# Performance work log

Measured on AMD Instinct MI355X. Metric: run time of the kernel, lower is better.

The kernel has to match this reference:

```python
import jax, jax.numpy as jnp
import numpy as np

# Model constants (match init_kwargs)
L = 32              # one_side_length (effective_L)
ED = 32             # embed_dim = n_ssm (repeat = 1)
ND = 2              # ndim
DIR = 4             # directions_amount
KD = DIR * ED       # kernel_dim = 128
R = 2 * L ** 3      # coeff_matrix_row_amount = 65536
V = 2 * L           # power_dim = 64
SCALE = (1.0 / ND) ** 0.5
B_IMG, H_IMG = 8, 64


def setup_inputs() -> dict:
    key = jax.random.key(0)
    ks = jax.random.split(key, 24)
    inp = {}
    inp['x'] = jax.random.normal(ks[0], (B_IMG, H_IMG, H_IMG, ED), jnp.float32)
    i = 1
    for d in ('h', 'v'):
        for s in ('A1', 'A2', 'A3', 'A4'):
            inp[f'M{d}_{s}'] = jax.random.uniform(ks[i], (R, V), jnp.float32); i += 1
        inp[f'M{d}_B'] = jax.random.uniform(ks[i], (R, 2), jnp.float32); i += 1
    for p in ('A_1', 'A_2', 'A_3', 'A_4', 'B_1', 'B_2', 'C_1', 'C_2'):
        inp[p] = jax.random.normal(ks[i], (KD, ND), jnp.float32); i += 1
    inp['W'] = jax.random.normal(ks[i], (ED, ED), jnp.float32); i += 1
    inp['b'] = jnp.zeros((ED,), jnp.float32)
    return inp


def _compute_kernel(Ms_h, Ms_v, A_list, B_1, B_2, C_1, C_2):
    # A powers via exp/log trick: [V, KD, ND]
    ell = jnp.arange(V, dtype=jnp.float32)
    Apow = [jnp.exp(ell[:, None, None] * jnp.log(jax.nn.sigmoid(a))[None]) for a in A_list]
    Bstk = jnp.stack([jax.nn.sigmoid(B_1), jax.nn.sigmoid(B_2)], 0)  # [2, KD, ND]
    vecs = Apow + [Bstk]
    outs = []
    for Ms in (Ms_h, Ms_v):
        prod = None
        for M, vec in zip(Ms, vecs):
            cur = jnp.einsum('rv,vhn->rhn', M, vec)  # [R, KD, ND]
            prod = cur if prod is None else prod * cur
        # [L^2, R/L^2, KD, ND] -> sum over r2 -> [L^2, KD, ND]
        outs.append(prod.reshape(L * L, R // (L * L), KD, ND).sum(axis=1))
    out = (jnp.einsum('lhn,hn->lh', outs[0], C_1 * SCALE)
           + jnp.einsum('lhn,hn->lh', outs[1], C_2 * SCALE))
    out = out.reshape(L, L, KD)
    # boundary corrections (first row/col doubled, corner net-unchanged)
    out = out.at[0, :, :].multiply(2.0)
    out = out.at[:, 0, :].multiply(2.0)
    out = out.at[0, 0].divide(4.0)
    return out  # [L, L, KD]


def _forward(x, Ms_h, Ms_v, A_list, B_1, B_2, C_1, C_2, W, b):
    xc = jnp.transpose(x, (0, 3, 1, 2))  # b c h w  (transpose=True path)
    H = xc.shape[-1]
    k = jnp.transpose(_compute_kernel(Ms_h, Ms_v, A_list, B_1, B_2, C_1, C_2), (2, 0, 1))  # [KD, L, L]
    pad = H - L
    k = jnp.pad(k, ((0, 0), (0, pad), (0, pad)))  # [KD, H, H]
    s2 = (2 * H, 2 * H)
    flips = [(), (2,), (3,), (2, 3)]
    y = None
    for i, fl in enumerate(flips):
        ki = k[i * ED:(i + 1) * ED]  # [ED, H, H] (repeat == 1)
        xi = jnp.flip(xc, fl) if fl else xc
        xf = jnp.fft.rfft2(xi, s=s2)
        kf = jnp.fft.rfft2(ki, s=s2)
        cur = jnp.fft.irfft2(xf * kf, s=s2)[..., :H, :H]
        cur = jnp.flip(cur, fl) if fl else cur
        y = cur if y is None else y + cur
    y = jnp.transpose(y, (0, 2, 3, 1))  # b h w c
    return y @ W.T + b  # mixing linear layer on channels


def reference(x, Mh_A1, Mh_A2, Mh_A3, Mh_A4, Mh_B,
              Mv_A1, Mv_A2, Mv_A3, Mv_A4, Mv_B,
              A_1, A_2, A_3, A_4, B_1, B_2, C_1, C_2, W, b):
    Ms_h = (Mh_A1, Mh_A2, Mh_A3, Mh_A4, Mh_B)
    Ms_v = (Mv_A1, Mv_A2, Mv_A3, Mv_A4, Mv_B)
    return _forward(x, Ms_h, Ms_v, [A_1, A_2, A_3, A_4], B_1, B_2, C_1, C_2, W, b)
```

## Files before the change

### kernel.cpp

```cpp
#include <hip/hip_runtime.h>
#include <hip/hip_fp16.h>

typedef _Float16 f16x8 __attribute__((ext_vector_type(8)));
typedef _Float16 half4v __attribute__((ext_vector_type(4)));
typedef float float4v __attribute__((ext_vector_type(4)));
typedef __attribute__((ext_vector_type(8))) short short8;
typedef __attribute__((ext_vector_type(16))) float f32x16;

#define WS_BFH   0
#define WS_BSG   65536
#define WS_OUTS  66048
#define WS_KC    590336
#define WS_XPAD  719360
#define WS_YC    1767936
#define WS_TF    2816512

__device__ inline unsigned short f2bf(float f) {
  unsigned int u = __float_as_uint(f);
  u += 0x7fffu + ((u >> 16) & 1u);
  return (unsigned short)(u >> 16);
}

__global__ void k0_prep(const float* __restrict__ A1, const float* __restrict__ A2,
                        const float* __restrict__ A3, const float* __restrict__ A4,
                        const float* __restrict__ B1, const float* __restrict__ B2,
                        _Float16* __restrict__ Bfh, float* __restrict__ bsg) {
  const int blk = blockIdx.x;
  const int i = blk >> 1, kb = blk & 1;
  const int hn = threadIdx.x;
  const float* As[4] = {A1, A2, A3, A4};
  const float a = As[i][hn];
  const float s = 1.0f / (1.0f + expf(-a));
  float p = 1.0f;
  for (int v = 0; v < kb * 32; ++v) p *= s;
  const int ntile = hn >> 4;
  #pragma unroll
  for (int g = 0; g < 4; ++g) {
    _Float16 h[8];
    #pragma unroll
    for (int j = 0; j < 8; ++j) { h[j] = (_Float16)p; p *= s; }
    const int lane = (hn & 15) | (g << 4);
    _Float16* dst = Bfh + ((((i * 2 + kb) * 16 + ntile) * 64 + lane) << 3);
    *(f16x8*)dst = *(f16x8*)h;
  }
  if (blk == 0) {
    bsg[hn]       = 1.0f / (1.0f + expf(-B1[hn]));
    bsg[256 + hn] = 1.0f / (1.0f + expf(-B2[hn]));
  }
}

__global__ __launch_bounds__(256, 4) void k1_mfma(
    const float* __restrict__ Mh0, const float* __restrict__ Mh1,
    const float* __restrict__ Mh2, const float* __restrict__ Mh3,
    const float* __restrict__ MhB,
    const float* __restrict__ Mv0, const float* __restrict__ Mv1,
    const float* __restrict__ Mv2, const float* __restrict__ Mv3,
    const float* __restrict__ MvB,
    const _Float16* __restrict__ Bfh, const float* __restrict__ bsg,
    float* __restrict__ outs) {
  __shared__ _Float16 Alds[4 * 4 * 2 * 64 * 8];
  __shared__ float MBs[128];
  __shared__ float bsgs[512];

  const int bd = blockIdx.x >> 10;
  const int l  = blockIdx.x & 1023;
  const float* Ms[4] = {bd ? Mv0 : Mh0, bd ? Mv1 : Mh1, bd ? Mv2 : Mh2, bd ? Mv3 : Mh3};
  const float* MB    = bd ? MvB : MhB;
  const int t = threadIdx.x;

  if (t < 128) MBs[t] = MB[l * 128 + t];
  bsgs[t]       = bsg[t];
  bsgs[256 + t] = bsg[256 + t];

  float4 st[16];
  #pragma unroll
  for (int i = 0; i < 4; ++i) {
    const float* M = Ms[i] + l * 4096;
    #pragma unroll
    for (int c0 = 0; c0 < 4; ++c0) {
      const int c = t + c0 * 256;
      st[i * 4 + c0] = *(const float4*)(M + ((c >> 4) * 64) + ((c & 15) << 2));
    }
  }
  #pragma unroll
  for (int i = 0; i < 4; ++i)
    #pragma unroll
    for (int c0 = 0; c0 < 4; ++c0) {
      const int c = t + c0 * 256;
      const int row = c >> 4;
      const int v4  = (c & 15) << 2;
      const int m     = row >> 4;
      const int lane2 = (row & 15) | (((v4 >> 3) & 3) << 4);
      const int kb    = v4 >> 5;
      const int jj    = v4 & 7;
      const float4 f = st[i * 4 + c0];
      half4v* dst = (half4v*)&Alds[((((i * 4 + m) * 2 + kb) * 64 + lane2) << 3) + jj];
      *dst = (half4v){(_Float16)f.x, (_Float16)f.y, (_Float16)f.z, (_Float16)f.w};
    }
  __syncthreads();

  const int w    = t >> 6;
  const int lane = t & 63;
  const int q = lane >> 4, col = lane & 15;

  #pragma unroll
  for (int half = 0; half < 2; ++half) {
    float4v E[4][2];
    #pragma unroll
    for (int i = 0; i < 4; ++i) {
      float4v acc[4][2];
      #pragma unroll
      for (int m = 0; m < 4; ++m)
        #pragma unroll
        for (int n = 0; n < 2; ++n) acc[m][n] = (float4v){0.f, 0.f, 0.f, 0.f};
      f16x8 Bf[2][2];
      #pragma unroll
      for (int kb = 0; kb < 2; ++kb)
        #pragma unroll
        for (int n = 0; n < 2; ++n)
          Bf[kb][n] = *(const f16x8*)(Bfh +
              ((((i * 2 + kb) * 16 + (w * 4 + half * 2 + n)) * 64 + lane) << 3));
      #pragma unroll
      for (int kb = 0; kb < 2; ++kb)
        #pragma unroll
        for (int m = 0; m < 4; ++m) {
          const f16x8 Af = *(const f16x8*)&Alds[((((i * 4 + m) * 2 + kb) * 64 + lane) << 3)];
          #pragma unroll
          for (int n = 0; n < 2; ++n)
            acc[m][n] = __builtin_amdgcn_mfma_f32_16x16x32_f16(Af, Bf[kb][n], acc[m][n], 0, 0, 0);
        }
      if (i == 0) {
        #pragma unroll
        for (int m = 0; m < 4; ++m)
          #pragma unroll
          for (int n = 0; n < 2; ++n) E[m][n] = acc[m][n];
      } else {
        #pragma unroll
        for (int m = 0; m < 4; ++m)
          #pragma unroll
          for (int n = 0; n < 2; ++n) E[m][n] *= acc[m][n];
      }
    }

    #pragma unroll
    for (int n = 0; n < 2; ++n) {
      const int hn = w * 64 + (half * 2 + n) * 16 + col;
      const float b0 = bsgs[hn], b1 = bsgs[256 + hn];
      float ssum = 0.f;
      #pragma unroll
      for (int m = 0; m < 4; ++m)
        #pragma unroll
        for (int r = 0; r < 4; ++r) {
          const int row = m * 16 + q * 4 + r;
          const float bdot = MBs[row * 2] * b0 + MBs[row * 2 + 1] * b1;
          ssum = fmaf(E[m][n][r], bdot, ssum);
        }
      ssum += __shfl_xor(ssum, 16);
      ssum += __shfl_xor(ssum, 32);
      if (lane < 16) outs[(bd * 1024 + l) * 256 + hn] = ssum;
    }
  }
}

__global__ void k2_kc(const float* __restrict__ outs, const float* __restrict__ C1,
                      const float* __restrict__ C2, float* __restrict__ kc) {
  const int c = blockIdx.x >> 3;
  const int base = (blockIdx.x & 7) * 504;
  const float SC = 0.70710678118654752f;
  for (int idx = base + threadIdx.x; idx < base + 504 && idx < 63 * 64; idx += 256) {
    const int U = idx >> 6, V = idx & 63;
    float acc = 0.f;
    if (V < 63) {
      const int u = U - 31, v = V - 31;
      #pragma unroll
      for (int d = 0; d < 4; ++d) {
        const int dy = (d == 1 || d == 3) ? u : -u;
        const int dx = (d == 2 || d == 3) ? v : -v;
        if (dy >= 0 && dy < 32 && dx >= 0 && dx < 32) {
          const int l = dy * 32 + dx;
          const int h = d * 32 + c;
          const float e = (dy == 0 && dx == 0) ? 1.f : ((dy == 0 || dx == 0) ? 2.f : 1.f);
          const float s0 = outs[l * 256 + h * 2 + 0] * C1[h * 2 + 0]
                         + outs[l * 256 + h * 2 + 1] * C1[h * 2 + 1];
          const float s1 = outs[262144 + l * 256 + h * 2 + 0] * C2[h * 2 + 0]
                         + outs[262144 + l * 256 + h * 2 + 1] * C2[h * 2 + 1];
          acc += e * SC * (s0 + s1);
        }
      }
    }
    kc[(c * 63 + U) * 64 + V] = acc;
  }
}

__global__ void k2b_tfrag(const float* __restrict__ kc, unsigned short* __restrict__ Tf) {
  const int cu = blockIdx.x;
  const float* kcr = kc + cu * 64;
  const int t = threadIdx.x;
  #pragma unroll
  for (int s = 0; s < 2; ++s) {
    const int slot = t + s * 256;
    const int f = slot >> 6, lane = slot & 63;
    const int kt = f >> 1, nt = f & 1;
    const int kbase = kt * 16 + (lane >> 5) * 8;
    const int n = nt * 32 + (lane & 31);
    unsigned int o[4];
    #pragma unroll
    for (int jp = 0; jp < 4; ++jp) {
      unsigned short h0, h1;
      {
        const int v = (kbase + 2 * jp) - n + 31;
        h0 = (v >= 0 && v < 63) ? f2bf(kcr[v]) : 0;
      }
      {
        const int v = (kbase + 2 * jp + 1) - n + 31;
        h1 = (v >= 0 && v < 63) ? f2bf(kcr[v]) : 0;
      }
      o[jp] = (unsigned int)h0 | ((unsigned int)h1 << 16);
    }
    unsigned int* dst = (unsigned int*)(Tf + (cu * 8 + f) * 512 + lane * 8);
    dst[0] = o[0]; dst[1] = o[1]; dst[2] = o[2]; dst[3] = o[3];
  }
}

__global__ void k3_xt(const float* __restrict__ x, unsigned short* __restrict__ Xpad) {
  __shared__ float ls[4 * 64 * 33];
  const int b = blockIdx.x >> 4, pt = blockIdx.x & 15;
  const int t = threadIdx.x;
  const float* src = x + (b * 64 + pt * 4) * 2048;
  #pragma unroll 8
  for (int k = 0; k < 32; ++k) {
    const int e = t + k * 256;
    const int p = e >> 11, q = (e >> 5) & 63, cl = e & 31;
    ls[(p * 64 + q) * 33 + cl] = src[e];
  }
  unsigned int* Xp32 = (unsigned int*)Xpad;
  for (int idx = blockIdx.x * 3968 + t; idx < (blockIdx.x + 1) * 3968; idx += 256) {
    const int seg = idx / 992, off = idx - seg * 992;
    const int bb = seg >> 6, cc = (seg >> 1) & 31, hf = seg & 1;
    Xp32[(bb * 32 + cc) * 4032 + (hf ? 3040 : 0) + off] = 0u;
  }
  __syncthreads();
  #pragma unroll 8
  for (int k = 0; k < 16; ++k) {
    const int o = t + k * 256;
    const int cl = o >> 7, p = (o >> 5) & 3, q2 = o & 31;
    const float f0 = ls[(p * 64 + 2 * q2 + 0) * 33 + cl];
    const float f1 = ls[(p * 64 + 2 * q2 + 1) * 33 + cl];
    const unsigned int pk = (unsigned int)f2bf(f0) | ((unsigned int)f2bf(f1) << 16);
    Xp32[(b * 32 + cl) * 4032 + (pt * 4 + p + 31) * 32 + q2] = pk;
  }
}

__global__ __launch_bounds__(256, 2) void k4b_conv(const unsigned short* __restrict__ Xpad,
                                                   const unsigned short* __restrict__ Tf,
                                                   float* __restrict__ yc) {
  __shared__ float red[4 * 4096];
  const int bc = blockIdx.x;
  const int c  = bc & 31;
  const int t = threadIdx.x, w = t >> 6, lane = t & 63;
  const unsigned short* Xp = Xpad + bc * 8064;
  const unsigned short* Tc = Tf + c * 63 * 4096;
  const int r = lane & 31, kh = lane >> 5;

  f32x16 acc[2][2];
  #pragma unroll
  for (int m = 0; m < 2; ++m)
    #pragma unroll
    for (int n = 0; n < 2; ++n)
      #pragma unroll
      for (int e = 0; e < 16; ++e) acc[m][n][e] = 0.f;

  short8 Ac[2][4], Bc[4][2];
  int u = w;
  #pragma unroll
  for (int m = 0; m < 2; ++m)
    #pragma unroll
    for (int kt = 0; kt < 4; ++kt)
      Ac[m][kt] = *(const short8*)(Xp + (m * 32 + r + u) * 64 + kt * 16 + kh * 8);
  #pragma unroll
  for (int kt = 0; kt < 4; ++kt)
    #pragma unroll
    for (int nt = 0; nt < 2; ++nt)
      Bc[kt][nt] = *(const short8*)(Tc + (u * 8 + kt * 2 + nt) * 512 + lane * 8);

  for (int i = 0; i < 16; ++i) {
    const int un = u + 4;
    const bool has_next = (un < 63);
    short8 An[2][4], Bn[4][2];
    if (has_next) {
      #pragma unroll
      for (int m = 0; m < 2; ++m)
        #pragma unroll
        for (int kt = 0; kt < 4; ++kt)
          An[m][kt] = *(const short8*)(Xp + (m * 32 + r + un) * 64 + kt * 16 + kh * 8);
      #pragma unroll
      for (int kt = 0; kt < 4; ++kt)
        #pragma unroll
        for (int nt = 0; nt < 2; ++nt)
          Bn[kt][nt] = *(const short8*)(Tc + (un * 8 + kt * 2 + nt) * 512 + lane * 8);
    }
    #pragma unroll
    for (int kt = 0; kt < 4; ++kt)
      #pragma unroll
      for (int m = 0; m < 2; ++m)
        #pragma unroll
        for (int nt = 0; nt < 2; ++nt)
          acc[m][nt] = __builtin_amdgcn_mfma_f32_32x32x16_bf16(Ac[m][kt], Bc[kt][nt],
                                                               acc[m][nt], 0, 0, 0);
    if (!has_next) break;
    #pragma unroll
    for (int m = 0; m < 2; ++m)
      #pragma unroll
      for (int kt = 0; kt < 4; ++kt) Ac[m][kt] = An[m][kt];
    #pragma unroll
    for (int kt = 0; kt < 4; ++kt)
      #pragma unroll
      for (int nt = 0; nt < 2; ++nt) Bc[kt][nt] = Bn[kt][nt];
    u = un;
  }

  float* my = red + w * 4096;
  #pragma unroll
  for (int m = 0; m < 2; ++m)
    #pragma unroll
    for (int nt = 0; nt < 2; ++nt)
      #pragma unroll
      for (int e = 0; e < 16; ++e) {
        const int row = (e & 3) + 8 * (e >> 2) + 4 * kh;
        my[(m * 32 + row) * 64 + nt * 32 + r] = acc[m][nt][e];
      }
  __syncthreads();
  float* out = yc + bc * 4096;
  #pragma unroll
  for (int k = 0; k < 16; ++k) {
    const int idx = t + k * 256;
    out[idx] = red[idx] + red[4096 + idx] + red[8192 + idx] + red[12288 + idx];
  }
}

__global__ void k5_out(const float* __restrict__ yc, const float* __restrict__ W,
                       const float* __restrict__ bias, float* __restrict__ out) {
  __shared__ float ysh[64 * 33];
  const int b = blockIdx.x >> 6, p = blockIdx.x & 63;
  const int t = threadIdx.x;
  const float* ybp = yc + b * 131072 + p * 64;
  #pragma unroll
  for (int k = 0; k < 8; ++k) {
    const int f = t + k * 256;
    const int cch = f >> 6, q = f & 63;
    ysh[q * 33 + cch] = ybp[cch * 4096 + q];
  }
  const int e = t & 31;
  float wr[32];
  #pragma unroll
  for (int c4 = 0; c4 < 8; ++c4) {
    const float4 f4 = *(const float4*)(W + e * 32 + c4 * 4);
    wr[c4 * 4 + 0] = f4.x; wr[c4 * 4 + 1] = f4.y;
    wr[c4 * 4 + 2] = f4.z; wr[c4 * 4 + 3] = f4.w;
  }
  const float bb = bias[e];
  __syncthreads();
  const int q0 = t >> 5;
  #pragma unroll
  for (int k = 0; k < 8; ++k) {
    const int q = q0 + k * 8;
    float a = bb;
    #pragma unroll
    for (int cc = 0; cc < 32; ++cc) a = fmaf(ysh[q * 33 + cc], wr[cc], a);
    out[((b * 64 + p) * 64 + q) * 32 + e] = a;
  }
}

extern "C" void kernel_launch(void* const* d_in, const int* in_sizes, int n_in,
                              void* d_out, int out_size, void* d_ws, size_t ws_size,
                              hipStream_t stream) {
  const float* x   = (const float*)d_in[0];
  const float* Mh[5] = {(const float*)d_in[1], (const float*)d_in[2], (const float*)d_in[3],
                        (const float*)d_in[4], (const float*)d_in[5]};
  const float* Mv[5] = {(const float*)d_in[6], (const float*)d_in[7], (const float*)d_in[8],
                        (const float*)d_in[9], (const float*)d_in[10]};
  const float* A1 = (const float*)d_in[11];
  const float* A2 = (const float*)d_in[12];
  const float* A3 = (const float*)d_in[13];
  const float* A4 = (const float*)d_in[14];
  const float* B1 = (const float*)d_in[15];
  const float* B2 = (const float*)d_in[16];
  const float* C1 = (const float*)d_in[17];
  const float* C2 = (const float*)d_in[18];
  const float* W  = (const float*)d_in[19];
  const float* bb = (const float*)d_in[20];
  float* ws  = (float*)d_ws;
  _Float16* Bfh = (_Float16*)(ws + WS_BFH);
  float* bsg  = ws + WS_BSG;
  float* outs = ws + WS_OUTS;
  float* kc   = ws + WS_KC;
  unsigned short* Xpad = (unsigned short*)(ws + WS_XPAD);
  float* yc   = ws + WS_YC;
  unsigned short* Tf = (unsigned short*)(ws + WS_TF);

  k0_prep<<<8, 256, 0, stream>>>(A1, A2, A3, A4, B1, B2, Bfh, bsg);
  k3_xt<<<128, 256, 0, stream>>>(x, Xpad);
  k1_mfma<<<2048, 256, 0, stream>>>(Mh[0], Mh[1], Mh[2], Mh[3], Mh[4],
                                    Mv[0], Mv[1], Mv[2], Mv[3], Mv[4],
                                    Bfh, bsg, outs);
  k2_kc<<<256, 256, 0, stream>>>(outs, C1, C2, kc);
  k2b_tfrag<<<2016, 256, 0, stream>>>(kc, Tf);
  k4b_conv<<<256, 256, 0, stream>>>(Xpad, Tf, yc);
  k5_out<<<512, 256, 0, stream>>>(yc, W, bb, (float*)d_out);
}
```

Before: 253.7 us.

## Double-buffer M tiles in LDS and overlap global loads with MFMA

Replaces the up-front load of all four M matrices into a 32KB LDS tile with a two-slot 16KB ping-pong buffer. Each of the eight (half, i) steps prefetches the next M slice from global memory into registers while MFMAs run on the current slot. This cuts LDS use and register staging, which may raise occupancy and hide load latency. The cost is a barrier per step and reloading the M matrices twice, once per half.

```diff
diff --git a/kernel.cpp b/kernel.cpp
--- a/kernel.cpp
+++ b/kernel.cpp
@@ -58,7 +58,7 @@
     const float* __restrict__ MvB,
     const _Float16* __restrict__ Bfh, const float* __restrict__ bsg,
     float* __restrict__ outs) {
-  __shared__ _Float16 Alds[4 * 4 * 2 * 64 * 8];
+  __shared__ _Float16 Ai[2][4096];
   __shared__ float MBs[128];
   __shared__ float bsgs[512];
 
@@ -72,92 +72,106 @@
   bsgs[t]       = bsg[t];
   bsgs[256 + t] = bsg[256 + t];
 
-  float4 st[16];
-  #pragma unroll
-  for (int i = 0; i < 4; ++i) {
-    const float* M = Ms[i] + l * 4096;
-    #pragma unroll
-    for (int c0 = 0; c0 < 4; ++c0) {
-      const int c = t + c0 * 256;
-      st[i * 4 + c0] = *(const float4*)(M + ((c >> 4) * 64) + ((c & 15) << 2));
-    }
-  }
-  #pragma unroll
-  for (int i = 0; i < 4; ++i)
-    #pragma unroll
-    for (int c0 = 0; c0 < 4; ++c0) {
-      const int c = t + c0 * 256;
-      const int row = c >> 4;
-      const int v4  = (c & 15) << 2;
-      const int m     = row >> 4;
-      const int lane2 = (row & 15) | (((v4 >> 3) & 3) << 4);
-      const int kb    = v4 >> 5;
-      const int jj    = v4 & 7;
-      const float4 f = st[i * 4 + c0];
-      half4v* dst = (half4v*)&Alds[((((i * 4 + m) * 2 + kb) * 64 + lane2) << 3) + jj];
-      *dst = (half4v){(_Float16)f.x, (_Float16)f.y, (_Float16)f.z, (_Float16)f.w};
-    }
-  __syncthreads();
-
-  const int w    = t >> 6;
-  const int lane = t & 63;
+  const int w = t >> 6, lane = t & 63;
   const int q = lane >> 4, col = lane & 15;
 
-  #pragma unroll
-  for (int half = 0; half < 2; ++half) {
-    float4v E[4][2];
-    #pragma unroll
-    for (int i = 0; i < 4; ++i) {
-      float4v acc[4][2];
+  int loff[4];
+  #pragma unroll
+  for (int c0 = 0; c0 < 4; ++c0) {
+    const int c = t + c0 * 256;
+    const int row = c >> 4;
+    const int v4  = (c & 15) << 2;
+    loff[c0] = (((row >> 4) * 2 + (v4 >> 5)) * 64 +
+                ((row & 15) | (((v4 >> 3) & 3) << 4))) * 8 + (v4 & 7);
+  }
+  const int gbase = l * 4096 + t * 4;
+
+  {
+    float4 f[4];
+    #pragma unroll
+    for (int c0 = 0; c0 < 4; ++c0) f[c0] = *(const float4*)(Ms[0] + gbase + c0 * 1024);
+    #pragma unroll
+    for (int c0 = 0; c0 < 4; ++c0)
+      *(half4v*)&Ai[0][loff[c0]] =
+          (half4v){(_Float16)f[c0].x, (_Float16)f[c0].y, (_Float16)f[c0].z, (_Float16)f[c0].w};
+  }
+
+  float4v E[4][2];
+  #pragma unroll
+  for (int hi = 0; hi < 8; ++hi) {
+    const int half = hi >> 2, i = hi & 3;
+    __syncthreads();
+
+    float4 ldn[4];
+    if (hi < 7) {
+      const float* Mn = Ms[(hi + 1) & 3];
+      #pragma unroll
+      for (int c0 = 0; c0 < 4; ++c0) ldn[c0] = *(const float4*)(Mn + gbase + c0 * 1024);
+    }
+
+    f16x8 Bf[2][2];
+    #pragma unroll
+    for (int kb = 0; kb < 2; ++kb)
+      #pragma unroll
+      for (int n = 0; n < 2; ++n)
+        Bf[kb][n] = *(const f16x8*)(Bfh +
+            ((((i * 2 + kb) * 16 + (w * 4 + half * 2 + n)) * 64 + lane) << 3));
+
+    float4v acc[4][2];
+    #pragma unroll
+    for (int m = 0; m < 4; ++m)
+      #pragma unroll
+      for (int n = 0; n < 2; ++n) acc[m][n] = (float4v){0.f, 0.f, 0.f, 0.f};
+
+    const _Float16* Ab = &Ai[hi & 1][0];
+    #pragma unroll
+    for (int kb = 0; kb < 2; ++kb)
+      #pragma unroll
+      for (int m = 0; m < 4; ++m) {
+        const f16x8 Af = *(const f16x8*)&Ab[(((m * 2 + kb) * 64 + lane) << 3)];
+        #pragma unroll
+        for (int n = 0; n < 2; ++n)
+          acc[m][n] = __builtin_amdgcn_mfma_f32_16x16x32_f16(Af, Bf[kb][n], acc[m][n], 0, 0, 0);
+      }
+
+    if (i == 0) {
       #pragma unroll
       for (int m = 0; m < 4; ++m)
         #pragma unroll
-        for (int n = 0; n < 2; ++n) acc[m][n] = (float4v){0.f, 0.f, 0.f, 0.f};
-      f16x8 Bf[2][2];
-      #pragma unroll
-      for (int kb = 0; kb < 2; ++kb)
-        #pragma unroll
-        for (int n = 0; n < 2; ++n)
-          Bf[kb][n] = *(const f16x8*)(Bfh +
-              ((((i * 2 + kb) * 16 + (w * 4 + half * 2 + n)) * 64 + lane) << 3));
-      #pragma unroll
-      for (int kb = 0; kb < 2; ++kb)
-        #pragma unroll
-        for (int m = 0; m < 4; ++m) {
-          const f16x8 Af = *(const f16x8*)&Alds[((((i * 4 + m) * 2 + kb) * 64 + lane) << 3)];
-          #pragma unroll
-          for (int n = 0; n < 2; ++n)
-            acc[m][n] = __builtin_amdgcn_mfma_f32_16x16x32_f16(Af, Bf[kb][n], acc[m][n], 0, 0, 0);
-        }
-      if (i == 0) {
+        for (int n = 0; n < 2; ++n) E[m][n] = acc[m][n];
+    } else {
+      #pragma unroll
+      for (int m = 0; m < 4; ++m)
+        #pragma unroll
+        for (int n = 0; n < 2; ++n) E[m][n] *= acc[m][n];
+    }
+
+    if (hi < 7) {
+      #pragma unroll
+      for (int c0 = 0; c0 < 4; ++c0)
+        *(half4v*)&Ai[(hi + 1) & 1][loff[c0]] =
+            (half4v){(_Float16)ldn[c0].x, (_Float16)ldn[c0].y,
+                     (_Float16)ldn[c0].z, (_Float16)ldn[c0].w};
+    }
+
+    if (i == 3) {
+      #pragma unroll
+      for (int n = 0; n < 2; ++n) {
+        const int hn = w * 64 + (half * 2 + n) * 16 + col;
+        const float b0 = bsgs[hn], b1 = bsgs[256 + hn];
+        float ssum = 0.f;
         #pragma unroll
         for (int m = 0; m < 4; ++m)
           #pragma unroll
-          for (int n = 0; n < 2; ++n) E[m][n] = acc[m][n];
-      } else {
-        #pragma unroll
-        for (int m = 0; m < 4; ++m)
-          #pragma unroll
-          for (int n = 0; n < 2; ++n) E[m][n] *= acc[m][n];
-      }
-    }
-
-    #pragma unroll
-    for (int n = 0; n < 2; ++n) {
-      const int hn = w * 64 + (half * 2 + n) * 16 + col;
-      const float b0 = bsgs[hn], b1 = bsgs[256 + hn];
-      float ssum = 0.f;
-      #pragma unroll
-      for (int m = 0; m < 4; ++m)
-        #pragma unroll
-        for (int r = 0; r < 4; ++r) {
-          const int row = m * 16 + q * 4 + r;
-          const float bdot = MBs[row * 2] * b0 + MBs[row * 2 + 1] * b1;
-          ssum = fmaf(E[m][n][r], bdot, ssum);
-        }
-      ssum += __shfl_xor(ssum, 16);
-      ssum += __shfl_xor(ssum, 32);
-      if (lane < 16) outs[(bd * 1024 + l) * 256 + hn] = ssum;
+          for (int r = 0; r < 4; ++r) {
+            const int row = m * 16 + q * 4 + r;
+            const float bdot = MBs[row * 2] * b0 + MBs[row * 2 + 1] * b1;
+            ssum = fmaf(E[m][n][r], bdot, ssum);
+          }
+        ssum += __shfl_xor(ssum, 16);
+        ssum += __shfl_xor(ssum, 32);
+        if (lane < 16) outs[(bd * 1024 + l) * 256 + hn] = ssum;
+      }
     }
   }
 }
```

After: 262.1 us. +3.3%, slower.

## Load MFMA A-fragments directly from global memory, bypassing LDS staging

Applied to the files above, without the earlier changes.

The k1 kernel no longer stages the M coefficient matrices through shared memory. Each wave now loads its A fragments straight from global memory into registers, converts them to fp16 in registers, and computes all four N tiles in one pass instead of two halves. This removes the LDS write/read round trip and one barrier, and each wave issues the MFMAs for one i directly. In exchange every wave redundantly reads the same M rows (4x global/L2 traffic), register pressure rises, and the launch bound drops to 2 blocks per CU.

```diff
diff --git a/kernel.cpp b/kernel.cpp
--- a/kernel.cpp
+++ b/kernel.cpp
@@ -49,7 +49,7 @@
   }
 }
 
-__global__ __launch_bounds__(256, 4) void k1_mfma(
+__global__ __launch_bounds__(256, 2) void k1_mfma(
     const float* __restrict__ Mh0, const float* __restrict__ Mh1,
     const float* __restrict__ Mh2, const float* __restrict__ Mh3,
     const float* __restrict__ MhB,
@@ -58,7 +58,6 @@
     const float* __restrict__ MvB,
     const _Float16* __restrict__ Bfh, const float* __restrict__ bsg,
     float* __restrict__ outs) {
-  __shared__ _Float16 Alds[4 * 4 * 2 * 64 * 8];
   __shared__ float MBs[128];
   __shared__ float bsgs[512];
 
@@ -71,94 +70,74 @@
   if (t < 128) MBs[t] = MB[l * 128 + t];
   bsgs[t]       = bsg[t];
   bsgs[256 + t] = bsg[256 + t];
-
-  float4 st[16];
+  __syncthreads();
+
+  const int w = t >> 6, lane = t & 63;
+  const int g = lane >> 4, cc = lane & 15;
+
+  const int goff = (l * 64 + cc) * 64 + g * 8;
+
+  float4v E[4][4];
   #pragma unroll
   for (int i = 0; i < 4; ++i) {
-    const float* M = Ms[i] + l * 4096;
-    #pragma unroll
-    for (int c0 = 0; c0 < 4; ++c0) {
-      const int c = t + c0 * 256;
-      st[i * 4 + c0] = *(const float4*)(M + ((c >> 4) * 64) + ((c & 15) << 2));
+    const float* Mi = Ms[i] + goff;
+    float4 Ld[16];
+    #pragma unroll
+    for (int m = 0; m < 4; ++m)
+      #pragma unroll
+      for (int kb = 0; kb < 2; ++kb) {
+        Ld[m * 4 + kb * 2 + 0] = *(const float4*)(Mi + m * 1024 + kb * 32);
+        Ld[m * 4 + kb * 2 + 1] = *(const float4*)(Mi + m * 1024 + kb * 32 + 4);
+      }
+    f16x8 Bf[2][4];
+    #pragma unroll
+    for (int kb = 0; kb < 2; ++kb)
+      #pragma unroll
+      for (int n = 0; n < 4; ++n)
+        Bf[kb][n] = *(const f16x8*)(Bfh +
+            ((((i * 2 + kb) * 16 + (w * 4 + n)) * 64 + lane) << 3));
+
+    #pragma unroll
+    for (int m = 0; m < 4; ++m) {
+      const float4 a = Ld[m * 4 + 0], b = Ld[m * 4 + 1];
+      const float4 c = Ld[m * 4 + 2], d = Ld[m * 4 + 3];
+      const f16x8 A0 = {(_Float16)a.x, (_Float16)a.y, (_Float16)a.z, (_Float16)a.w,
+                        (_Float16)b.x, (_Float16)b.y, (_Float16)b.z, (_Float16)b.w};
+      const f16x8 A1 = {(_Float16)c.x, (_Float16)c.y, (_Float16)c.z, (_Float16)c.w,
+                        (_Float16)d.x, (_Float16)d.y, (_Float16)d.z, (_Float16)d.w};
+      float4v tn[4];
+      #pragma unroll
+      for (int n = 0; n < 4; ++n) {
+        tn[n] = __builtin_amdgcn_mfma_f32_16x16x32_f16(A0, Bf[0][n],
+                                                       (float4v){0.f, 0.f, 0.f, 0.f}, 0, 0, 0);
+        tn[n] = __builtin_amdgcn_mfma_f32_16x16x32_f16(A1, Bf[1][n], tn[n], 0, 0, 0);
+      }
+      if (i == 0) {
+        #pragma unroll
+        for (int n = 0; n < 4; ++n) E[m][n] = tn[n];
+      } else {
+        #pragma unroll
+        for (int n = 0; n < 4; ++n) E[m][n] *= tn[n];
+      }
     }
   }
-  #pragma unroll
-  for (int i = 0; i < 4; ++i)
-    #pragma unroll
-    for (int c0 = 0; c0 < 4; ++c0) {
-      const int c = t + c0 * 256;
-      const int row = c >> 4;
-      const int v4  = (c & 15) << 2;
-      const int m     = row >> 4;
-      const int lane2 = (row & 15) | (((v4 >> 3) & 3) << 4);
-      const int kb    = v4 >> 5;
-      const int jj    = v4 & 7;
-      const float4 f = st[i * 4 + c0];
-      half4v* dst = (half4v*)&Alds[((((i * 4 + m) * 2 + kb) * 64 + lane2) << 3) + jj];
-      *dst = (half4v){(_Float16)f.x, (_Float16)f.y, (_Float16)f.z, (_Float16)f.w};
-    }
-  __syncthreads();
-
-  const int w    = t >> 6;
-  const int lane = t & 63;
-  const int q = lane >> 4, col = lane & 15;
-
-  #pragma unroll
-  for (int half = 0; half < 2; ++half) {
-    float4v E[4][2];
-    #pragma unroll
-    for (int i = 0; i < 4; ++i) {
-      float4v acc[4][2];
-      #pragma unroll
-      for (int m = 0; m < 4; ++m)
-        #pragma unroll
-        for (int n = 0; n < 2; ++n) acc[m][n] = (float4v){0.f, 0.f, 0.f, 0.f};
-      f16x8 Bf[2][2];
-      #pragma unroll
-      for (int kb = 0; kb < 2; ++kb)
-        #pragma unroll
-        for (int n = 0; n < 2; ++n)
-          Bf[kb][n] = *(const f16x8*)(Bfh +
-              ((((i * 2 + kb) * 16 + (w * 4 + half * 2 + n)) * 64 + lane) << 3));
-      #pragma unroll
-      for (int kb = 0; kb < 2; ++kb)
-        #pragma unroll
-        for (int m = 0; m < 4; ++m) {
-          const f16x8 Af = *(const f16x8*)&Alds[((((i * 4 + m) * 2 + kb) * 64 + lane) << 3)];
-          #pragma unroll
-          for (int n = 0; n < 2; ++n)
-            acc[m][n] = __builtin_amdgcn_mfma_f32_16x16x32_f16(Af, Bf[kb][n], acc[m][n], 0, 0, 0);
-        }
-      if (i == 0) {
-        #pragma unroll
-        for (int m = 0; m < 4; ++m)
-          #pragma unroll
-          for (int n = 0; n < 2; ++n) E[m][n] = acc[m][n];
-      } else {
-        #pragma unroll
-        for (int m = 0; m < 4; ++m)
-          #pragma unroll
-          for (int n = 0; n < 2; ++n) E[m][n] *= acc[m][n];
-      }
-    }
-
-    #pragma unroll
-    for (int n = 0; n < 2; ++n) {
-      const int hn = w * 64 + (half * 2 + n) * 16 + col;
-      const float b0 = bsgs[hn], b1 = bsgs[256 + hn];
-      float ssum = 0.f;
-      #pragma unroll
-      for (int m = 0; m < 4; ++m)
-        #pragma unroll
-        for (int r = 0; r < 4; ++r) {
-          const int row = m * 16 + q * 4 + r;
-          const float bdot = MBs[row * 2] * b0 + MBs[row * 2 + 1] * b1;
-          ssum = fmaf(E[m][n][r], bdot, ssum);
-        }
-      ssum += __shfl_xor(ssum, 16);
-      ssum += __shfl_xor(ssum, 32);
-      if (lane < 16) outs[(bd * 1024 + l) * 256 + hn] = ssum;
-    }
+
+  #pragma unroll
+  for (int n = 0; n < 4; ++n) {
+    const int hn = w * 64 + n * 16 + cc;
+    const float b0 = bsgs[hn], b1 = bsgs[256 + hn];
+    float ssum = 0.f;
+    #pragma unroll
+    for (int m = 0; m < 4; ++m)
+      #pragma unroll
+      for (int r = 0; r < 4; ++r) {
+        const int row = m * 16 + g * 4 + r;
+        const float bdot = MBs[row * 2] * b0 + MBs[row * 2 + 1] * b1;
+        ssum = fmaf(E[m][n][r], bdot, ssum);
+      }
+    ssum += __shfl_xor(ssum, 16);
+    ssum += __shfl_xor(ssum, 32);
+    if (lane < 16) outs[(bd * 1024 + l) * 256 + hn] = ssum;
   }
 }
 
```

Result: slower. 285.2 us (+12.4%).
